# Kernel optimization log

Measured on AMD Instinct MI355X. Metric: run time of the kernel, lower is better.

Reference implementation:

```python
import jax, jax.numpy as jnp
import numpy as np

D = 4096          # input_dim == output_dim (square FAUST factors)
N = 1024          # batch rows of U
NNZ = 131072      # nonzeros per factor (32 per row)
K = 4             # number of sparse factors


def setup_inputs() -> dict:
    key = jax.random.key(0)
    k_u, k_b, k_v, k_r, k_c = jax.random.split(key, 5)
    U = jax.random.normal(k_u, (N, D), dtype=jnp.float32)
    bias = jax.random.normal(k_b, (D,), dtype=jnp.float32)
    # glorot-ish scaling: ~32 nnz per row -> scale by 1/sqrt(32) for stable chain
    vals = jax.random.normal(k_v, (K, NNZ), dtype=jnp.float32) * (1.0 / np.sqrt(32.0))
    rows = jax.random.randint(k_r, (K, NNZ), 0, D, dtype=jnp.int32)
    cols = jax.random.randint(k_c, (K, NNZ), 0, D, dtype=jnp.int32)
    return {"U": U, "bias": bias, "vals": vals, "rows": rows, "cols": cols}


def _spmm(rows, cols, vals, X):
    # sparse (COO) [D, D] @ dense X [D, N] -> [D, N]
    return jax.ops.segment_sum(vals[:, None] * X[cols], rows, num_segments=D)


def reference(U, bias, vals, rows, cols):
    # torch code applies sparse_matrices[-1] first, then [k-2] ... [0]
    y = U.T  # [D, N]
    for i in range(K - 1, -1, -1):
        y = _spmm(rows[i], cols[i], vals[i], y)
    return y.T + bias  # [N, D]
```

## Files before the change

kernel.cpp:

```cpp
#include <hip/hip_runtime.h>

#define D_DIM 4096
#define N_DIM 1024
#define NNZ_F 131072
#define K_F 4
#define NCHUNK 8
#define LPR 16
#define RPB 16
#define MAXE 1024
#define XS8 (N_DIM / 8)

#define T_TILES ((D_DIM / 64) * (N_DIM / 64))
#define TSTRIDE 132

__device__ __forceinline__ unsigned short f2bf(float f) {
    union { float f; unsigned int u; } v; v.f = f;
    unsigned int r = v.u + 0x7fffu + ((v.u >> 16) & 1u);
    return (unsigned short)(r >> 16);
}
__device__ __forceinline__ float bf_lo(unsigned int w) {
    return __uint_as_float(w << 16);
}
__device__ __forceinline__ float bf_hi(unsigned int w) {
    return __uint_as_float(w & 0xffff0000u);
}

__global__ __launch_bounds__(1024) void fused_t_build_k(const float* __restrict__ in,
                                                        unsigned short* __restrict__ outb,
                                                        const int* __restrict__ rows,
                                                        int* __restrict__ row_ptr_g,
                                                        int* __restrict__ cursor_g) {
    __shared__ int s_cnt[4 * D_DIM];
    __shared__ int s_part[1024];
    const int tid = threadIdx.x;
    const int bid = blockIdx.x;

    if (bid < T_TILES) {
        float (*tile)[65] = (float (*)[65])s_cnt;
        const int gxi = bid & 63;
        const int gyi = bid >> 6;
        const int c0 = gxi * 64;
        const int r0 = gyi * 64;
        const int tx = tid & 63;
        const int ty = tid >> 6;
#pragma unroll
        for (int i = ty; i < 64; i += 16)
            tile[i][tx] = in[(size_t)(r0 + i) * D_DIM + c0 + tx];
        __syncthreads();
        const int px = (tid & 15) * 4;
        const int py = tid >> 4;
        ushort4 w;
        w.x = f2bf(tile[px + 0][py]);
        w.y = f2bf(tile[px + 1][py]);
        w.z = f2bf(tile[px + 2][py]);
        w.w = f2bf(tile[px + 3][py]);
        *(ushort4*)&outb[(size_t)(c0 + py) * N_DIM + r0 + px] = w;
        return;
    }

    const int f = bid - T_TILES;
    const int grp = (tid >> 8) & 3;
#pragma unroll
    for (int k = 0; k < 16; ++k) s_cnt[tid + k * 1024] = 0;
    __syncthreads();

    int* h = s_cnt + grp * D_DIM;
    const int4* rp4 = (const int4*)(rows + (size_t)f * NNZ_F);
#pragma unroll 4
    for (int it = 0; it < NNZ_F / 4096; ++it) {
        int4 r4 = rp4[(size_t)it * 1024 + tid];
        atomicAdd(&h[r4.x], 1);
        atomicAdd(&h[r4.y], 1);
        atomicAdd(&h[r4.z], 1);
        atomicAdd(&h[r4.w], 1);
    }
    __syncthreads();

    int c[4];
#pragma unroll
    for (int k = 0; k < 4; ++k)
        c[k] = s_cnt[tid * 4 + k] + s_cnt[D_DIM + tid * 4 + k]
             + s_cnt[2 * D_DIM + tid * 4 + k] + s_cnt[3 * D_DIM + tid * 4 + k];
    const int part = c[0] + c[1] + c[2] + c[3];
    s_part[tid] = part;
    __syncthreads();
    for (int off = 1; off < 1024; off <<= 1) {
        int v = (tid >= off) ? s_part[tid - off] : 0;
        __syncthreads();
        s_part[tid] += v;
        __syncthreads();
    }
    int excl = s_part[tid] - part;

    int* rp  = row_ptr_g + (size_t)f * (D_DIM + 1);
    int* cur = cursor_g + (size_t)f * D_DIM;
    int b = tid * 4;
#pragma unroll
    for (int k = 0; k < 4; ++k) {
        rp[b + k] = excl; cur[b + k] = excl; excl += c[k];
    }
    if (tid == 1023) rp[D_DIM] = NNZ_F;
}

__global__ __launch_bounds__(1024) void scatter_all_k(const int* __restrict__ rows,
                                                      const int* __restrict__ cols,
                                                      const float* __restrict__ vals,
                                                      int* __restrict__ cursor,
                                                      int* __restrict__ csr_col,
                                                      float* __restrict__ csr_val) {
    const int f = blockIdx.x >> 7;
    const size_t j = (size_t)(blockIdx.x & 127) * 1024 + threadIdx.x;
    const size_t base = (size_t)f * NNZ_F;
    int r = rows[base + j];
    int p = atomicAdd(&cursor[(size_t)f * D_DIM + r], 1);
    csr_col[base + p] = cols[base + j];
    csr_val[base + p] = vals[base + j];
}

template <bool FINAL>
__global__ __launch_bounds__(256) void spmm_chunk_k(const int* __restrict__ row_ptr,
                                                    const int* __restrict__ csr_col,
                                                    const float* __restrict__ csr_val,
                                                    const char* __restrict__ Xb,
                                                    uint4* __restrict__ Y,
                                                    float* __restrict__ out,
                                                    const float* __restrict__ bias) {
    __shared__ float smem[16 * TSTRIDE];
    int*   s_col = (int*)smem;
    float* s_val = smem + MAXE;
    int*   s_ptr = (int*)(smem + 2 * MAXE);

    const int tid   = threadIdx.x;
    const int chunk = blockIdx.x & (NCHUNK - 1);
    const int rg    = blockIdx.x >> 3;
    const int r0    = rg * RPB;
    const int sub   = tid >> 4;
    const int lane  = tid & 15;
    const int slot  = chunk * LPR + lane;
    const unsigned sl16 = (unsigned)slot * 16u;
    const int r     = r0 + sub;

    if (tid <= RPB) s_ptr[tid] = row_ptr[r0 + tid];
    __syncthreads();
    const int base  = s_ptr[0];
    const int total = s_ptr[RPB] - base;
    const int start = s_ptr[sub] - base;
    const int end_  = s_ptr[sub + 1] - base;

    float acc[8];
#pragma unroll
    for (int k = 0; k < 8; ++k) acc[k] = 0.f;

    for (int cb2 = 0; cb2 < total; cb2 += MAXE) {
        int cnt = total - cb2;
        if (cnt > MAXE) cnt = MAXE;
        for (int t = tid; t < cnt; t += 256) {
            s_col[t] = csr_col[base + cb2 + t];
            s_val[t] = csr_val[base + cb2 + t];
        }
        __syncthreads();
        const int js = start > cb2 ? start : cb2;
        const int je = end_ < cb2 + cnt ? end_ : cb2 + cnt;
        int j = js;
#pragma unroll 2
        for (; j + 1 < je; j += 2) {
            const int j0 = j - cb2;
            const unsigned o0 = ((unsigned)s_col[j0] << 11) + sl16;
            const unsigned o1 = ((unsigned)s_col[j0 + 1] << 11) + sl16;
            const uint4 x0 = *(const uint4*)(Xb + o0);
            const uint4 x1 = *(const uint4*)(Xb + o1);
            const float v0 = s_val[j0];
            const float v1 = s_val[j0 + 1];
            acc[0] += v0 * bf_lo(x0.x); acc[1] += v0 * bf_hi(x0.x);
            acc[2] += v0 * bf_lo(x0.y); acc[3] += v0 * bf_hi(x0.y);
            acc[4] += v0 * bf_lo(x0.z); acc[5] += v0 * bf_hi(x0.z);
            acc[6] += v0 * bf_lo(x0.w); acc[7] += v0 * bf_hi(x0.w);
            acc[0] += v1 * bf_lo(x1.x); acc[1] += v1 * bf_hi(x1.x);
            acc[2] += v1 * bf_lo(x1.y); acc[3] += v1 * bf_hi(x1.y);
            acc[4] += v1 * bf_lo(x1.z); acc[5] += v1 * bf_hi(x1.z);
            acc[6] += v1 * bf_lo(x1.w); acc[7] += v1 * bf_hi(x1.w);
        }
        if (j < je) {
            const int j0 = j - cb2;
            const unsigned o0 = ((unsigned)s_col[j0] << 11) + sl16;
            const uint4 x0 = *(const uint4*)(Xb + o0);
            const float v0 = s_val[j0];
            acc[0] += v0 * bf_lo(x0.x); acc[1] += v0 * bf_hi(x0.x);
            acc[2] += v0 * bf_lo(x0.y); acc[3] += v0 * bf_hi(x0.y);
            acc[4] += v0 * bf_lo(x0.z); acc[5] += v0 * bf_hi(x0.z);
            acc[6] += v0 * bf_lo(x0.w); acc[7] += v0 * bf_hi(x0.w);
        }
        __syncthreads();
    }

    if (!FINAL) {
        uint4 o;
        o.x = (unsigned int)f2bf(acc[0]) | ((unsigned int)f2bf(acc[1]) << 16);
        o.y = (unsigned int)f2bf(acc[2]) | ((unsigned int)f2bf(acc[3]) << 16);
        o.z = (unsigned int)f2bf(acc[4]) | ((unsigned int)f2bf(acc[5]) << 16);
        o.w = (unsigned int)f2bf(acc[6]) | ((unsigned int)f2bf(acc[7]) << 16);
        Y[(size_t)r * XS8 + slot] = o;
    } else {
        __syncthreads();
        float* tile = smem;
        const int wbase = sub * TSTRIDE + lane * 8;
        *(float4*)&tile[wbase]     = make_float4(acc[0], acc[1], acc[2], acc[3]);
        *(float4*)&tile[wbase + 4] = make_float4(acc[4], acc[5], acc[6], acc[7]);
        __syncthreads();
        const int n0 = chunk * (N_DIM / NCHUNK);
#pragma unroll
        for (int t = tid; t < 512; t += 256) {
            const int n_loc = t >> 2;
            const int q     = t & 3;
            float4 o;
            o.x = tile[(q * 4 + 0) * TSTRIDE + n_loc];
            o.y = tile[(q * 4 + 1) * TSTRIDE + n_loc];
            o.z = tile[(q * 4 + 2) * TSTRIDE + n_loc];
            o.w = tile[(q * 4 + 3) * TSTRIDE + n_loc];
            const float4 bv = *(const float4*)&bias[r0 + q * 4];
            o.x += bv.x; o.y += bv.y; o.z += bv.z; o.w += bv.w;
            *(float4*)&out[(size_t)(n0 + n_loc) * D_DIM + r0 + q * 4] = o;
        }
    }
}

extern "C" void kernel_launch(void* const* d_in, const int* in_sizes, int n_in,
                              void* d_out, int out_size, void* d_ws, size_t ws_size,
                              hipStream_t stream) {
    const float* U    = (const float*)d_in[0];
    const float* bias = (const float*)d_in[1];
    const float* vals = (const float*)d_in[2];
    const int*   rows = (const int*)d_in[3];
    const int*   cols = (const int*)d_in[4];
    float* out = (float*)d_out;

    char* ws = (char*)d_ws;
    size_t off = 0;
    char* bufA = ws;                   off += (size_t)D_DIM * N_DIM * 2;
    char* bufB = ws + off;             off += (size_t)D_DIM * N_DIM * 2;
    int* row_ptr = (int*)(ws + off);   off += (size_t)K_F * (D_DIM + 1) * 4;
    off = (off + 15) & ~(size_t)15;
    int* cursor  = (int*)(ws + off);   off += (size_t)K_F * D_DIM * 4;
    int*   csr_col = (int*)(ws + off); off += (size_t)K_F * NNZ_F * 4;
    float* csr_val = (float*)(ws + off); off += (size_t)K_F * NNZ_F * 4;

    const int grid_spmm = (D_DIM / RPB) * NCHUNK;

    fused_t_build_k<<<T_TILES + K_F, 1024, 0, stream>>>(
        U, (unsigned short*)bufA, rows, row_ptr, cursor);

    scatter_all_k<<<K_F * (NNZ_F / 1024), 1024, 0, stream>>>(rows, cols, vals, cursor,
                                                             csr_col, csr_val);

    spmm_chunk_k<false><<<grid_spmm, 256, 0, stream>>>(
        row_ptr + 3 * (D_DIM + 1), csr_col + 3 * (size_t)NNZ_F, csr_val + 3 * (size_t)NNZ_F,
        (const char*)bufA, (uint4*)bufB, nullptr, nullptr);
    spmm_chunk_k<false><<<grid_spmm, 256, 0, stream>>>(
        row_ptr + 2 * (D_DIM + 1), csr_col + 2 * (size_t)NNZ_F, csr_val + 2 * (size_t)NNZ_F,
        (const char*)bufB, (uint4*)bufA, nullptr, nullptr);
    spmm_chunk_k<false><<<grid_spmm, 256, 0, stream>>>(
        row_ptr + 1 * (D_DIM + 1), csr_col + 1 * (size_t)NNZ_F, csr_val + 1 * (size_t)NNZ_F,
        (const char*)bufA, (uint4*)bufB, nullptr, nullptr);
    spmm_chunk_k<true><<<grid_spmm, 256, 0, stream>>>(
        row_ptr + 0 * (D_DIM + 1), csr_col + 0 * (size_t)NNZ_F, csr_val + 0 * (size_t)NNZ_F,
        (const char*)bufB, nullptr, out, bias);
}
```

Measured before the change: 111.3 us.

## Sort rows by nonzero count for balanced SpMM blocks in intermediate factors

For factors 1–3, the CSR build now does an in-block counting sort of rows by nonzero count. It emits a permuted row_ptr and a sorted_rows map, so each 16-row SpMM block processes rows of similar length. The SpMM kernel reads the real output row from this map. The aim is to cut intra-block imbalance, where sub-groups with short rows sit idle while the longest row finishes. It also moves the four build blocks to the front of the fused grid so they get scheduled early. The cost is extra shared-memory histogram work and scans in the build kernel, one more index load per SpMM block, and output rows that are no longer written in order.

Result: no change. 111.2 us (-0.1%).

```diff
diff --git a/kernel.cpp b/kernel.cpp
--- a/kernel.cpp
+++ b/kernel.cpp
@@ -29,16 +29,18 @@
                                                         unsigned short* __restrict__ outb,
                                                         const int* __restrict__ rows,
                                                         int* __restrict__ row_ptr_g,
-                                                        int* __restrict__ cursor_g) {
+                                                        int* __restrict__ cursor_g,
+                                                        int* __restrict__ srow_g) {
     __shared__ int s_cnt[4 * D_DIM];
     __shared__ int s_part[1024];
     const int tid = threadIdx.x;
     const int bid = blockIdx.x;
 
-    if (bid < T_TILES) {
+    if (bid >= K_F) {
+        const int tb = bid - K_F;
         float (*tile)[65] = (float (*)[65])s_cnt;
-        const int gxi = bid & 63;
-        const int gyi = bid >> 6;
+        const int gxi = tb & 63;
+        const int gyi = tb >> 6;
         const int c0 = gxi * 64;
         const int r0 = gyi * 64;
         const int tx = tid & 63;
@@ -58,7 +60,7 @@
         return;
     }
 
-    const int f = bid - T_TILES;
+    const int f = bid;
     const int grp = (tid >> 8) & 3;
 #pragma unroll
     for (int k = 0; k < 16; ++k) s_cnt[tid + k * 1024] = 0;
@@ -81,23 +83,62 @@
     for (int k = 0; k < 4; ++k)
         c[k] = s_cnt[tid * 4 + k] + s_cnt[D_DIM + tid * 4 + k]
              + s_cnt[2 * D_DIM + tid * 4 + k] + s_cnt[3 * D_DIM + tid * 4 + k];
-    const int part = c[0] + c[1] + c[2] + c[3];
-    s_part[tid] = part;
-    __syncthreads();
-    for (int off = 1; off < 1024; off <<= 1) {
-        int v = (tid >= off) ? s_part[tid - off] : 0;
-        __syncthreads();
-        s_part[tid] += v;
-        __syncthreads();
-    }
-    int excl = s_part[tid] - part;
-
-    int* rp  = row_ptr_g + (size_t)f * (D_DIM + 1);
-    int* cur = cursor_g + (size_t)f * D_DIM;
-    int b = tid * 4;
+    const int b = tid * 4;
+
+    int*   rp   = row_ptr_g + (size_t)f * (D_DIM + 1);
+    int*   cur  = cursor_g + (size_t)f * D_DIM;
+    int*   srow = srow_g + (size_t)f * D_DIM;
+
+    if (f == 0) {
+        const int part = c[0] + c[1] + c[2] + c[3];
+        s_part[tid] = part;
+        __syncthreads();
+        for (int off = 1; off < 1024; off <<= 1) {
+            int v = (tid >= off) ? s_part[tid - off] : 0;
+            __syncthreads();
+            s_part[tid] += v;
+            __syncthreads();
+        }
+        int excl = s_part[tid] - part;
+#pragma unroll
+        for (int k = 0; k < 4; ++k) {
+            rp[b + k] = excl; cur[b + k] = excl; srow[b + k] = b + k; excl += c[k];
+        }
+        if (tid == 1023) rp[D_DIM] = NNZ_F;
+        return;
+    }
+
+    __syncthreads();
+    int* hist = s_cnt + 4096;
+    int* binc = s_cnt + 4352;
+    int* sA   = s_cnt + 4608;
+    int* sB   = s_cnt + 4864;
+    if (tid < 256) { hist[tid] = 0; binc[tid] = 0; }
+    __syncthreads();
 #pragma unroll
     for (int k = 0; k < 4; ++k) {
-        rp[b + k] = excl; cur[b + k] = excl; excl += c[k];
+        int l = c[k] > 255 ? 255 : c[k];
+        atomicAdd(&hist[l], 1);
+    }
+    __syncthreads();
+    if (tid < 256) { int hv = hist[tid]; sA[tid] = hv; sB[tid] = hv * tid; }
+    __syncthreads();
+    for (int off = 1; off < 256; off <<= 1) {
+        int a = 0, bb = 0;
+        if (tid < 256 && tid >= off) { a = sA[tid - off]; bb = sB[tid - off]; }
+        __syncthreads();
+        if (tid < 256) { sA[tid] += a; sB[tid] += bb; }
+        __syncthreads();
+    }
+#pragma unroll
+    for (int k = 0; k < 4; ++k) {
+        const int l = c[k] > 255 ? 255 : c[k];
+        const int idx = atomicAdd(&binc[l], 1);
+        const int pos    = sA[l] - hist[l] + idx;
+        const int startp = sB[l] - hist[l] * l + idx * l;
+        srow[pos] = b + k;
+        rp[pos] = startp;
+        cur[b + k] = startp;
     }
     if (tid == 1023) rp[D_DIM] = NNZ_F;
 }
@@ -119,6 +160,7 @@
 
 template <bool FINAL>
 __global__ __launch_bounds__(256) void spmm_chunk_k(const int* __restrict__ row_ptr,
+                                                    const int* __restrict__ sorted_rows,
                                                     const int* __restrict__ csr_col,
                                                     const float* __restrict__ csr_val,
                                                     const char* __restrict__ Xb,
@@ -126,9 +168,10 @@
                                                     float* __restrict__ out,
                                                     const float* __restrict__ bias) {
     __shared__ float smem[16 * TSTRIDE];
-    int*   s_col = (int*)smem;
-    float* s_val = smem + MAXE;
-    int*   s_ptr = (int*)(smem + 2 * MAXE);
+    int*   s_col  = (int*)smem;
+    float* s_val  = smem + MAXE;
+    int*   s_ptr  = (int*)(smem + 2 * MAXE);
+    int*   s_srow = (int*)(smem + 2 * MAXE + 32);
 
     const int tid   = threadIdx.x;
     const int chunk = blockIdx.x & (NCHUNK - 1);
@@ -138,14 +181,15 @@
     const int lane  = tid & 15;
     const int slot  = chunk * LPR + lane;
     const unsigned sl16 = (unsigned)slot * 16u;
-    const int r     = r0 + sub;
 
     if (tid <= RPB) s_ptr[tid] = row_ptr[r0 + tid];
+    if (tid < RPB)  s_srow[tid] = sorted_rows[r0 + tid];
     __syncthreads();
     const int base  = s_ptr[0];
     const int total = s_ptr[RPB] - base;
     const int start = s_ptr[sub] - base;
     const int end_  = s_ptr[sub + 1] - base;
+    const int r     = s_srow[sub];
 
     float acc[8];
 #pragma unroll
@@ -241,27 +285,32 @@
     int* row_ptr = (int*)(ws + off);   off += (size_t)K_F * (D_DIM + 1) * 4;
     off = (off + 15) & ~(size_t)15;
     int* cursor  = (int*)(ws + off);   off += (size_t)K_F * D_DIM * 4;
+    int* srow    = (int*)(ws + off);   off += (size_t)K_F * D_DIM * 4;
     int*   csr_col = (int*)(ws + off); off += (size_t)K_F * NNZ_F * 4;
     float* csr_val = (float*)(ws + off); off += (size_t)K_F * NNZ_F * 4;
 
     const int grid_spmm = (D_DIM / RPB) * NCHUNK;
 
     fused_t_build_k<<<T_TILES + K_F, 1024, 0, stream>>>(
-        U, (unsigned short*)bufA, rows, row_ptr, cursor);
+        U, (unsigned short*)bufA, rows, row_ptr, cursor, srow);
 
     scatter_all_k<<<K_F * (NNZ_F / 1024), 1024, 0, stream>>>(rows, cols, vals, cursor,
                                                              csr_col, csr_val);
 
     spmm_chunk_k<false><<<grid_spmm, 256, 0, stream>>>(
-        row_ptr + 3 * (D_DIM + 1), csr_col + 3 * (size_t)NNZ_F, csr_val + 3 * (size_t)NNZ_F,
+        row_ptr + 3 * (D_DIM + 1), srow + 3 * D_DIM,
+        csr_col + 3 * (size_t)NNZ_F, csr_val + 3 * (size_t)NNZ_F,
         (const char*)bufA, (uint4*)bufB, nullptr, nullptr);
     spmm_chunk_k<false><<<grid_spmm, 256, 0, stream>>>(
-        row_ptr + 2 * (D_DIM + 1), csr_col + 2 * (size_t)NNZ_F, csr_val + 2 * (size_t)NNZ_F,
+        row_ptr + 2 * (D_DIM + 1), srow + 2 * D_DIM,
+        csr_col + 2 * (size_t)NNZ_F, csr_val + 2 * (size_t)NNZ_F,
         (const char*)bufB, (uint4*)bufA, nullptr, nullptr);
     spmm_chunk_k<false><<<grid_spmm, 256, 0, stream>>>(
-        row_ptr + 1 * (D_DIM + 1), csr_col + 1 * (size_t)NNZ_F, csr_val + 1 * (size_t)NNZ_F,
+        row_ptr + 1 * (D_DIM + 1), srow + 1 * D_DIM,
+        csr_col + 1 * (size_t)NNZ_F, csr_val + 1 * (size_t)NNZ_F,
         (const char*)bufA, (uint4*)bufB, nullptr, nullptr);
     spmm_chunk_k<true><<<grid_spmm, 256, 0, stream>>>(
-        row_ptr + 0 * (D_DIM + 1), csr_col + 0 * (size_t)NNZ_F, csr_val + 0 * (size_t)NNZ_F,
+        row_ptr + 0 * (D_DIM + 1), srow + 0 * D_DIM,
+        csr_col + 0 * (size_t)NNZ_F, csr_val + 0 * (size_t)NNZ_F,
         (const char*)bufB, nullptr, out, bias);
 }
```
